# Performance work log

Measured on AMD Instinct MI355X. Metric: run time of the kernel, lower is better.

The kernel has to match this reference:

```python
import jax, jax.numpy as jnp
import numpy as np

WELL_WIDTH = 0.5   # morse_well_width (length scale of the well)
WELL_DEPTH = 1.0   # morse_well_depth (energy scale)
N = 4096
BOX = 100.0


def setup_inputs() -> dict:
    key = jax.random.key(0)
    k1, k2, k3 = jax.random.split(key, 3)
    position = jax.random.uniform(k1, (N, 3), minval=0.0, maxval=BOX, dtype=jnp.float32)
    radius = jax.random.uniform(k2, (N,), minval=0.5, maxval=1.5, dtype=jnp.float32)
    active = jax.random.bernoulli(k3, 0.9, (N,))
    return {"position": position, "radius": radius, "active": active}


def reference(position, radius, active):
    # All-pairs Morse force: V(r) = D * (exp(-2(r-r0)/w) - 2*exp(-(r-r0)/w)),
    # F_i = -dV/dr * (x_i - x_j)/r summed over active j != i, with r0 = rad_i + rad_j.
    n = position.shape[0]
    dx = position[:, None, :] - position[None, :, :]          # [N, N, 3]
    dist2 = jnp.sum(dx * dx, axis=-1)                         # [N, N]
    eye = jnp.eye(n, dtype=bool)
    mask = active[:, None] & active[None, :] & ~eye           # [N, N]
    r = jnp.sqrt(jnp.where(mask, dist2, 1.0))                 # safe sqrt (no 0 at diag)
    r0 = radius[:, None] + radius[None, :]                    # rest distance
    e = jnp.exp(-(r - r0) / WELL_WIDTH)
    # force magnitude along the separation direction: -dV/dr
    mag = (2.0 * WELL_DEPTH / WELL_WIDTH) * (e * e - e)       # [N, N]
    mag = jnp.where(mask, mag, 0.0)
    force = jnp.sum((mag / r)[..., None] * dx, axis=1)        # [N, 3]
    return force
```

## Files before the change

kernel.cpp:

```cpp
#include <hip/hip_runtime.h>


constexpr int   NN     = 4096;
constexpr int   BLOCK  = 256;
constexpr int   JCHUNK = 64;
constexpr float KEXP   = 2.8853900817779268f;

static __device__ __forceinline__ float fast_rsq(float x) {
    float r;
    asm("v_rsq_f32 %0, %1" : "=v"(r) : "v"(x));
    return r;
}
static __device__ __forceinline__ float fast_exp2(float x) {
    float r;
    asm("v_exp_f32 %0, %1" : "=v"(r) : "v"(x));
    return r;
}

__global__ __launch_bounds__(BLOCK) void morse_force_kernel(
    const float* __restrict__ pos,
    const float* __restrict__ rad,
    const int*   __restrict__ act,
    float*       __restrict__ out)
{
    __shared__ float4 sj[JCHUNK];

    const int tid = threadIdx.x;
    const int i   = blockIdx.x * BLOCK + tid;
    const int j0  = blockIdx.y * JCHUNK;

    const float xi  = pos[3*i+0];
    const float yi  = pos[3*i+1];
    const float zi  = pos[3*i+2];
    const float kri = KEXP * rad[i];
    const int   ai  = act[i];

    if (tid < JCHUNK) {
        const int j = j0 + tid;
        const float sw = act[j] ? (KEXP * rad[j]) : -1e30f;
        sj[tid] = make_float4(pos[3*j+0], pos[3*j+1], pos[3*j+2], sw);
    }
    __syncthreads();

    float fx = 0.f, fy = 0.f, fz = 0.f;

    #pragma unroll 16
    for (int t = 0; t < JCHUNK; ++t) {
        const float4 p = sj[t];
        const float dx = xi - p.x;
        const float dy = yi - p.y;
        const float dz = zi - p.z;
        const float d2 = fmaf(dx, dx, fmaf(dy, dy, dz * dz));

        const float irv = fast_rsq(d2);
        const float r   = d2 * irv;
        const float arg = fmaf(-KEXP, r, kri + p.w);
        const float e   = fast_exp2(arg);
        const float em  = fmaf(e, e, -e);
        float s = em * irv;
        if (j0 + t == i) s = 0.f;

        fx = fmaf(s, dx, fx);
        fy = fmaf(s, dy, fy);
        fz = fmaf(s, dz, fz);
    }

    if (ai) {
        atomicAdd(&out[3*i+0], 4.f * fx);
        atomicAdd(&out[3*i+1], 4.f * fy);
        atomicAdd(&out[3*i+2], 4.f * fz);
    }
}

extern "C" void kernel_launch(void* const* d_in, const int* in_sizes, int n_in,
                              void* d_out, int out_size, void* d_ws, size_t ws_size,
                              hipStream_t stream) {
    const float* pos = (const float*)d_in[0];
    const float* rad = (const float*)d_in[1];
    const int*   act = (const int*)d_in[2];
    float*       out = (float*)d_out;

    hipMemsetAsync(d_out, 0, (size_t)out_size * sizeof(float), stream);

    dim3 grid(NN / BLOCK, NN / JCHUNK);
    morse_force_kernel<<<grid, BLOCK, 0, stream>>>(pos, rad, act, out);
}
```

Before: 73.17 us.

## Assign each block four particles and reduce partner sums in-block instead of atomics

Work is now split so each 256-thread block owns 4 i-particles, with 64 lanes per particle striding over all j. The j positions are staged through shared memory in 1024-element chunks, and per-lane partial forces are combined with wavefront shuffles and a small shared reduction. This removes the global atomics and the memset launch. In exchange every block reloads all 4096 j entries, so the j data is re-read 1024 times, and the grid shrinks to 1024 blocks.

```diff
diff --git a/kernel.cpp b/kernel.cpp
--- a/kernel.cpp
+++ b/kernel.cpp
@@ -3,7 +3,11 @@
 
 constexpr int   NN     = 4096;
 constexpr int   BLOCK  = 256;
-constexpr int   JCHUNK = 64;
+constexpr int   TI     = 4;
+constexpr int   SL     = BLOCK / TI;
+constexpr int   CHUNK  = 1024;
+constexpr int   NCHUNK = NN / CHUNK;
+constexpr int   IPC    = CHUNK / SL;
 constexpr float KEXP   = 2.8853900817779268f;
 
 static __device__ __forceinline__ float fast_rsq(float x) {
@@ -23,52 +27,83 @@
     const int*   __restrict__ act,
     float*       __restrict__ out)
 {
-    __shared__ float4 sj[JCHUNK];
+    __shared__ float4 sj[CHUNK];
+    __shared__ float  red[BLOCK/64][TI][3];
 
     const int tid = threadIdx.x;
-    const int i   = blockIdx.x * BLOCK + tid;
-    const int j0  = blockIdx.y * JCHUNK;
+    const int il  = tid & (TI - 1);
+    const int s   = tid >> 2;
+    const int i0  = blockIdx.x * TI;
+    const int i   = i0 + il;
 
     const float xi  = pos[3*i+0];
     const float yi  = pos[3*i+1];
     const float zi  = pos[3*i+2];
     const float kri = KEXP * rad[i];
-    const int   ai  = act[i];
 
-    if (tid < JCHUNK) {
-        const int j = j0 + tid;
-        const float sw = act[j] ? (KEXP * rad[j]) : -1e30f;
-        sj[tid] = make_float4(pos[3*j+0], pos[3*j+1], pos[3*j+2], sw);
+    float fx = 0.f, fy = 0.f, fz = 0.f;
+    int jv = s;
+
+    for (int c = 0; c < NCHUNK; ++c) {
+        #pragma unroll
+        for (int u = 0; u < CHUNK / BLOCK; ++u) {
+            const int jj = tid + BLOCK * u;
+            const int j  = c * CHUNK + jj;
+            const float sw = act[j] ? (KEXP * rad[j]) : -1e30f;
+            sj[jj] = make_float4(pos[3*j+0], pos[3*j+1], pos[3*j+2], sw);
+        }
+        __syncthreads();
+
+        #pragma unroll
+        for (int kk = 0; kk < IPC; ++kk) {
+            const float4 p = sj[s + SL * kk];
+            const float dx = xi - p.x;
+            const float dy = yi - p.y;
+            const float dz = zi - p.z;
+            const float d2 = fmaf(dx, dx, fmaf(dy, dy, dz * dz));
+
+            const float irv = fast_rsq(d2);
+            const float r   = d2 * irv;
+            const float arg = fmaf(-KEXP, r, kri + p.w);
+            const float e   = fast_exp2(arg);
+            const float em  = fmaf(e, e, -e);
+            float sc = em * irv;
+            if (jv == i) sc = 0.f;
+
+            fx = fmaf(sc, dx, fx);
+            fy = fmaf(sc, dy, fy);
+            fz = fmaf(sc, dz, fz);
+            jv += SL;
+        }
+        __syncthreads();
+    }
+
+    #pragma unroll
+    for (int off = TI; off < 64; off <<= 1) {
+        fx += __shfl_xor(fx, off, 64);
+        fy += __shfl_xor(fy, off, 64);
+        fz += __shfl_xor(fz, off, 64);
+    }
+    const int w = tid >> 6;
+    if ((tid & 63) < TI) {
+        red[w][il][0] = fx;
+        red[w][il][1] = fy;
+        red[w][il][2] = fz;
     }
     __syncthreads();
-
-    float fx = 0.f, fy = 0.f, fz = 0.f;
-
-    #pragma unroll 16
-    for (int t = 0; t < JCHUNK; ++t) {
-        const float4 p = sj[t];
-        const float dx = xi - p.x;
-        const float dy = yi - p.y;
-        const float dz = zi - p.z;
-        const float d2 = fmaf(dx, dx, fmaf(dy, dy, dz * dz));
-
-        const float irv = fast_rsq(d2);
-        const float r   = d2 * irv;
-        const float arg = fmaf(-KEXP, r, kri + p.w);
-        const float e   = fast_exp2(arg);
-        const float em  = fmaf(e, e, -e);
-        float s = em * irv;
-        if (j0 + t == i) s = 0.f;
-
-        fx = fmaf(s, dx, fx);
-        fy = fmaf(s, dy, fy);
-        fz = fmaf(s, dz, fz);
-    }
-
-    if (ai) {
-        atomicAdd(&out[3*i+0], 4.f * fx);
-        atomicAdd(&out[3*i+1], 4.f * fy);
-        atomicAdd(&out[3*i+2], 4.f * fz);
+    if (tid < TI) {
+        float sx = 0.f, sy = 0.f, sz = 0.f;
+        #pragma unroll
+        for (int ww = 0; ww < BLOCK / 64; ++ww) {
+            sx += red[ww][tid][0];
+            sy += red[ww][tid][1];
+            sz += red[ww][tid][2];
+        }
+        const int ii = i0 + tid;
+        const float scale = act[ii] ? 4.f : 0.f;
+        out[3*ii+0] = scale * sx;
+        out[3*ii+1] = scale * sy;
+        out[3*ii+2] = scale * sz;
     }
 }
 
@@ -80,8 +115,5 @@
     const int*   act = (const int*)d_in[2];
     float*       out = (float*)d_out;
 
-    hipMemsetAsync(d_out, 0, (size_t)out_size * sizeof(float), stream);
-
-    dim3 grid(NN / BLOCK, NN / JCHUNK);
-    morse_force_kernel<<<grid, BLOCK, 0, stream>>>(pos, rad, act, out);
+    morse_force_kernel<<<dim3(NN / TI), BLOCK, 0, stream>>>(pos, rad, act, out);
 }
```

Result: faster. 69.09 us (-5.6%).
